# Optimization experiments

Measured on AMD Instinct MI355X. Metric: run time of the kernel, lower is better.

The kernel has to match this reference:

```python
import jax, jax.numpy as jnp
import numpy as np


def setup_inputs() -> dict:
    key = jax.random.key(0)
    ks = jax.random.split(key, 6)
    N, E, D = 50000, 500000, 128
    H, O = 256, 128
    x = jax.random.normal(ks[0], (N, D), dtype=jnp.float32)
    edge_attr = jax.random.normal(ks[1], (E, D), dtype=jnp.float32)
    edge_index = jax.random.randint(ks[2], (E, 2), 0, N, dtype=jnp.int64)
    # MLP params, scaled like torch default init
    W1 = jax.random.normal(ks[3], (3 * D, H), dtype=jnp.float32) / np.sqrt(3 * D)
    b1 = jnp.zeros((H,), dtype=jnp.float32)
    W2 = jax.random.normal(ks[4], (H, O), dtype=jnp.float32) / np.sqrt(H)
    b2 = jnp.zeros((O,), dtype=jnp.float32)
    return {"x": x, "edge_attr": edge_attr, "W1": W1, "b1": b1,
            "W2": W2, "b2": b2, "edge_index": edge_index}


def reference(x, edge_attr, W1, b1, W2, b2, edge_index):
    # edge_index: [E, 2]; column 0 = sender, column 1 = receiver
    sender = x[edge_index[:, 0]]    # [E, D] gather
    receiver = x[edge_index[:, 1]]  # [E, D] gather
    feat = jnp.concatenate([sender, receiver, edge_attr], axis=-1)  # [E, 3D]
    h = jax.nn.relu(feat @ W1 + b1)  # [E, H]
    return h @ W2 + b2               # [E, O]
```

## Files before the change

kernel.cpp:

```cpp
#include <hip/hip_runtime.h>
#include <hip/hip_bf16.h>

#define D 128
#define K1 384
#define H 256
#define O 128
#define BE 64
#define GRIDP 256
#define LDF (K1 + 8)
#define LDHF (H + 8)

typedef __attribute__((ext_vector_type(8))) short bf16x8;
typedef __attribute__((ext_vector_type(4))) float f32x4;

#define SSW(row, col) ((row) * 128 + ((col) ^ (((row) & 15) << 3)))
#define HSW(row, col) ((row) * 256 + ((col) ^ (((row) & 15) << 3)))

#define LGKM_BARRIER()                                                 \
    do {                                                               \
        asm volatile("s_waitcnt lgkmcnt(0)\n\ts_barrier" ::: "memory");\
        __builtin_amdgcn_sched_barrier(0);                             \
    } while (0)

__device__ inline ushort f2b(float f) {
    union { float f; unsigned u; } v; v.f = f;
    unsigned u = v.u;
    unsigned r = (u + 0x7fffu + ((u >> 16) & 1u)) >> 16;
    return (ushort)r;
}
__device__ inline ushort4 cvt4(float4 v) {
    ushort4 u; u.x = f2b(v.x); u.y = f2b(v.y); u.z = f2b(v.z); u.w = f2b(v.w); return u;
}
__device__ inline unsigned cvtpk(float lo, float hi) {
    unsigned r;
    asm("v_cvt_pk_bf16_f32 %0, %1, %2" : "=v"(r) : "v"(lo), "v"(hi));
    return r;
}
__device__ inline bf16x8 cvt8(f32x4 a, f32x4 b) {
    union { bf16x8 v; unsigned w[4]; } u;
    u.w[0] = cvtpk(a[0], a[1]); u.w[1] = cvtpk(a[2], a[3]);
    u.w[2] = cvtpk(b[0], b[1]); u.w[3] = cvtpk(b[2], b[3]);
    return u.v;
}

__global__ void prep_weights(const float* __restrict__ W1, const float* __restrict__ W2,
                             ushort* __restrict__ W1t, ushort* __restrict__ W2t) {
    int tid = blockIdx.x * blockDim.x + threadIdx.x;
    if (tid < 256 * 384) {
        int n = tid / 384, k = tid % 384;
        W1t[tid] = f2b(W1[k * 256 + n]);
    } else {
        int t2 = tid - 256 * 384;
        if (t2 < 128 * 256) {
            int o = t2 / 256, k = t2 % 256;
            W2t[t2] = f2b(W2[k * 128 + o]);
        }
    }
}

__global__ __launch_bounds__(256)
void prep_x(const float* __restrict__ x, ushort* __restrict__ Xb, long total8) {
    long t = (long)blockIdx.x * blockDim.x + threadIdx.x;
    if (t < total8) {
        const float* src = x + t * 8;
        float4 v0 = ((const float4*)src)[0], v1 = ((const float4*)src)[1];
        union { bf16x8 v; ushort4 u[2]; } w;
        w.u[0] = cvt4(v0); w.u[1] = cvt4(v1);
        *(bf16x8*)(Xb + t * 8) = w.v;
    }
}

__global__ __launch_bounds__(512, 2)
void edge_mlp16(const float* __restrict__ ea, const int* __restrict__ eidx,
                const ushort* __restrict__ Xb,
                const ushort* __restrict__ W1t, const ushort* __restrict__ W2t,
                const float* __restrict__ b1, const float* __restrict__ b2,
                float* __restrict__ out, int E, int ntiles) {
    __shared__ __align__(16) ushort sBuf[65536];
    ushort* sH = sBuf + 49152;

    const int tid = threadIdx.x;
    const int wave = tid >> 6, lane = tid & 63;
    const int row16 = lane & 15, kgrp = lane >> 4;
    const int srow = tid >> 3, oct = tid & 7;

    bf16x8 w1f[12][2];
    #pragma unroll
    for (int ks = 0; ks < 12; ++ks)
        #pragma unroll
        for (int fc = 0; fc < 2; ++fc)
            w1f[ks][fc] = *(const bf16x8*)(W1t + (wave * 32 + fc * 16 + row16) * K1 + ks * 32 + kgrp * 8);
    bf16x8 w2f[8];
    #pragma unroll
    for (int ks = 0; ks < 8; ++ks)
        w2f[ks] = *(const bf16x8*)(W2t + (wave * 16 + row16) * H + ks * 32 + kgrp * 8);
    float4 b1q[2];
    #pragma unroll
    for (int fc = 0; fc < 2; ++fc)
        b1q[fc] = *(const float4*)(b1 + wave * 32 + fc * 16 + kgrp * 4);
    const float b2v = b2[wave * 16 + row16];

    int t = blockIdx.x;
    if (t >= ntiles) return;

    bf16x8 pxs[2], pxr[2];
    f32x4  pea[4];

    {
        long se = (long)t * BE + srow; if (se >= E) se = E - 1;
        int2 ei = *(const int2*)(eidx + 2 * se);
        const ushort* ps = Xb + (long)ei.x * D + oct * 16;
        const ushort* pr = Xb + (long)ei.y * D + oct * 16;
        const float*  pe = ea + se * D + oct * 16;
        #pragma unroll
        for (int j = 0; j < 2; ++j) pxs[j] = *(const bf16x8*)(ps + j * 8);
        #pragma unroll
        for (int j = 0; j < 2; ++j) pxr[j] = *(const bf16x8*)(pr + j * 8);
        #pragma unroll
        for (int j = 0; j < 4; ++j) pea[j] = ((const f32x4*)pe)[j];

        #pragma unroll
        for (int j = 0; j < 2; ++j) *(bf16x8*)(sBuf + SSW(srow, oct * 16 + j * 8)) = pxs[j];
        #pragma unroll
        for (int j = 0; j < 2; ++j) *(bf16x8*)(sBuf + 8192 + SSW(srow, oct * 16 + j * 8)) = pxr[j];
        *(bf16x8*)(sBuf + 16384 + SSW(srow, oct * 16 + 0)) = cvt8(pea[0], pea[1]);
        *(bf16x8*)(sBuf + 16384 + SSW(srow, oct * 16 + 8)) = cvt8(pea[2], pea[3]);
    }

    int p = 0;
    int tprev = -1;
    int tn = t + GRIDP;
    int2 ei2;
    {
        int tc = (tn < ntiles) ? tn : (ntiles - 1);
        long se = (long)tc * BE + srow; if (se >= E) se = E - 1;
        ei2 = *(const int2*)(eidx + 2 * se);
    }

    for (;;) {
        LGKM_BARRIER();
        const bool hasNext = (tn < ntiles);

        if (tprev >= 0) {
            f32x4 acc2[4];
            #pragma unroll
            for (int fr = 0; fr < 4; ++fr) acc2[fr] = (f32x4){0,0,0,0};
            #pragma unroll
            for (int ks = 0; ks < 8; ++ks) {
                bf16x8 a[4];
                #pragma unroll
                for (int fr = 0; fr < 4; ++fr)
                    a[fr] = *(const bf16x8*)(sH + HSW(fr * 16 + row16, ks * 32 + kgrp * 8));
                #pragma unroll
                for (int fr = 0; fr < 4; ++fr)
                    acc2[fr] = __builtin_amdgcn_mfma_f32_16x16x32_bf16(a[fr], w2f[ks], acc2[fr], 0, 0, 0);
            }
            const long e0p = (long)tprev * BE;
            #pragma unroll
            for (int fr = 0; fr < 4; ++fr)
                #pragma unroll
                for (int r = 0; r < 4; ++r) {
                    long erow = e0p + fr * 16 + kgrp * 4 + r;
                    if (erow < E) out[erow * O + wave * 16 + row16] = acc2[fr][r] + b2v;
                }
        }

        if (hasNext) {
            long sen = (long)tn * BE + srow; if (sen >= E) sen = E - 1;
            const ushort* ps = Xb + (long)ei2.x * D + oct * 16;
            const ushort* pr = Xb + (long)ei2.y * D + oct * 16;
            const float*  pe = ea + sen * D + oct * 16;
            #pragma unroll
            for (int j = 0; j < 2; ++j) pxs[j] = *(const bf16x8*)(ps + j * 8);
            #pragma unroll
            for (int j = 0; j < 2; ++j) pxr[j] = *(const bf16x8*)(pr + j * 8);
            #pragma unroll
            for (int j = 0; j < 4; ++j) pea[j] = ((const f32x4*)pe)[j];
            int tnn = tn + GRIDP;
            int tc = (tnn < ntiles) ? tnn : (ntiles - 1);
            long se2 = (long)tc * BE + srow; if (se2 >= E) se2 = E - 1;
            ei2 = *(const int2*)(eidx + 2 * se2);
        }

        const ushort* sA = sBuf + (p ? 24576 : 0);
        f32x4 acc[4][2];
        #pragma unroll
        for (int fe = 0; fe < 4; ++fe) { acc[fe][0] = (f32x4){0,0,0,0}; acc[fe][1] = (f32x4){0,0,0,0}; }
        #pragma unroll
        for (int ks = 0; ks < 12; ++ks) {
            const ushort* sP = sA + ((ks < 4) ? 0 : ((ks < 8) ? 8192 : 16384));
            const int kl = (ks & 3) * 32 + kgrp * 8;
            bf16x8 a[4];
            #pragma unroll
            for (int fe = 0; fe < 4; ++fe)
                a[fe] = *(const bf16x8*)(sP + SSW(fe * 16 + row16, kl));
            #pragma unroll
            for (int fe = 0; fe < 4; ++fe) {
                acc[fe][0] = __builtin_amdgcn_mfma_f32_16x16x32_bf16(w1f[ks][0], a[fe], acc[fe][0], 0, 0, 0);
                acc[fe][1] = __builtin_amdgcn_mfma_f32_16x16x32_bf16(w1f[ks][1], a[fe], acc[fe][1], 0, 0, 0);
            }
        }

        if (hasNext) {
            ushort* sB = sBuf + (p ? 0 : 24576);
            #pragma unroll
            for (int j = 0; j < 2; ++j) *(bf16x8*)(sB + SSW(srow, oct * 16 + j * 8)) = pxs[j];
            #pragma unroll
            for (int j = 0; j < 2; ++j) *(bf16x8*)(sB + 8192 + SSW(srow, oct * 16 + j * 8)) = pxr[j];
            *(bf16x8*)(sB + 16384 + SSW(srow, oct * 16 + 0)) = cvt8(pea[0], pea[1]);
            *(bf16x8*)(sB + 16384 + SSW(srow, oct * 16 + 8)) = cvt8(pea[2], pea[3]);
        }

        LGKM_BARRIER();

        #pragma unroll
        for (int fe = 0; fe < 4; ++fe) {
            int erow = fe * 16 + row16;
            int base = erow * 256;
            int swz = (erow & 15) << 3;
            #pragma unroll
            for (int fc = 0; fc < 2; ++fc) {
                int colb = wave * 32 + fc * 16 + kgrp * 4;
                union { uint2 w; ushort4 u; } pk;
                pk.w.x = cvtpk(fmaxf(acc[fe][fc][0] + b1q[fc].x, 0.f),
                               fmaxf(acc[fe][fc][1] + b1q[fc].y, 0.f));
                pk.w.y = cvtpk(fmaxf(acc[fe][fc][2] + b1q[fc].z, 0.f),
                               fmaxf(acc[fe][fc][3] + b1q[fc].w, 0.f));
                *(ushort4*)(sH + base + (colb ^ swz)) = pk.u;
            }
        }

        tprev = t; t = tn; tn += GRIDP;
        if (t >= ntiles) break;
        p ^= 1;
    }

    LGKM_BARRIER();
    {
        f32x4 acc2[4];
        #pragma unroll
        for (int fr = 0; fr < 4; ++fr) acc2[fr] = (f32x4){0,0,0,0};
        #pragma unroll
        for (int ks = 0; ks < 8; ++ks) {
            bf16x8 a[4];
            #pragma unroll
            for (int fr = 0; fr < 4; ++fr)
                a[fr] = *(const bf16x8*)(sH + HSW(fr * 16 + row16, ks * 32 + kgrp * 8));
            #pragma unroll
            for (int fr = 0; fr < 4; ++fr)
                acc2[fr] = __builtin_amdgcn_mfma_f32_16x16x32_bf16(a[fr], w2f[ks], acc2[fr], 0, 0, 0);
        }
        const long e0p = (long)tprev * BE;
        #pragma unroll
        for (int fr = 0; fr < 4; ++fr)
            #pragma unroll
            for (int r = 0; r < 4; ++r) {
                long erow = e0p + fr * 16 + kgrp * 4 + r;
                if (erow < E) out[erow * O + wave * 16 + row16] = acc2[fr][r] + b2v;
            }
    }
}

__global__ __launch_bounds__(256, 2)
void edge_mlp(const float* __restrict__ x, const float* __restrict__ ea,
              const int* __restrict__ eidx,
              const float* __restrict__ b1, const float* __restrict__ b2,
              const ushort* __restrict__ W1t, const ushort* __restrict__ W2t,
              float* __restrict__ out, int E) {
    __shared__ ushort sF[64 * LDF];
    ushort* sH = sF;
    const int tid = threadIdx.x, wave = tid >> 6, lane = tid & 63;
    const int row16 = lane & 15, kgrp = lane >> 4;
    const long e0 = (long)blockIdx.x * 64;
    {
        int i = tid >> 2, p = tid & 3;
        long e = e0 + i; if (e >= E) e = E - 1;
        int s = eidx[2 * e], r = eidx[2 * e + 1];
        const float* src0 = x + (long)s * D + p * 32;
        const float* src1 = x + (long)r * D + p * 32;
        const float* src2 = ea + e * D + p * 32;
        ushort* dst = sF + i * LDF + p * 32;
        #pragma unroll
        for (int j = 0; j < 8; ++j) *(ushort4*)(dst + 0 * D + j * 4) = cvt4(((const float4*)src0)[j]);
        #pragma unroll
        for (int j = 0; j < 8; ++j) *(ushort4*)(dst + 1 * D + j * 4) = cvt4(((const float4*)src1)[j]);
        #pragma unroll
        for (int j = 0; j < 8; ++j) *(ushort4*)(dst + 2 * D + j * 4) = cvt4(((const float4*)src2)[j]);
    }
    __syncthreads();
    f32x4 acc[4][4];
    #pragma unroll
    for (int a = 0; a < 4; ++a)
        #pragma unroll
        for (int b = 0; b < 4; ++b) acc[a][b] = (f32x4){0,0,0,0};
    const int wcol = wave * 64;
    for (int k0 = 0; k0 < K1; k0 += 32) {
        bf16x8 a[4], b[4];
        #pragma unroll
        for (int fr = 0; fr < 4; ++fr)
            a[fr] = *(const bf16x8*)(sF + (fr * 16 + row16) * LDF + k0 + kgrp * 8);
        #pragma unroll
        for (int fc = 0; fc < 4; ++fc)
            b[fc] = *(const bf16x8*)(W1t + (wcol + fc * 16 + row16) * K1 + k0 + kgrp * 8);
        #pragma unroll
        for (int fr = 0; fr < 4; ++fr)
            #pragma unroll
            for (int fc = 0; fc < 4; ++fc)
                acc[fr][fc] = __builtin_amdgcn_mfma_f32_16x16x32_bf16(a[fr], b[fc], acc[fr][fc], 0, 0, 0);
    }
    __syncthreads();
    #pragma unroll
    for (int fc = 0; fc < 4; ++fc) {
        int col = wcol + fc * 16 + row16;
        float bv = b1[col];
        #pragma unroll
        for (int fr = 0; fr < 4; ++fr)
            #pragma unroll
            for (int r = 0; r < 4; ++r) {
                int row = fr * 16 + kgrp * 4 + r;
                sH[row * LDHF + col] = f2b(fmaxf(acc[fr][fc][r] + bv, 0.f));
            }
    }
    __syncthreads();
    f32x4 acc2[4][2];
    #pragma unroll
    for (int a = 0; a < 4; ++a)
        #pragma unroll
        for (int b = 0; b < 2; ++b) acc2[a][b] = (f32x4){0,0,0,0};
    const int wo = wave * 32;
    for (int k0 = 0; k0 < H; k0 += 32) {
        bf16x8 a[4], b[2];
        #pragma unroll
        for (int fr = 0; fr < 4; ++fr)
            a[fr] = *(const bf16x8*)(sH + (fr * 16 + row16) * LDHF + k0 + kgrp * 8);
        #pragma unroll
        for (int fc = 0; fc < 2; ++fc)
            b[fc] = *(const bf16x8*)(W2t + (wo + fc * 16 + row16) * H + k0 + kgrp * 8);
        #pragma unroll
        for (int fr = 0; fr < 4; ++fr)
            #pragma unroll
            for (int fc = 0; fc < 2; ++fc)
                acc2[fr][fc] = __builtin_amdgcn_mfma_f32_16x16x32_bf16(a[fr], b[fc], acc2[fr][fc], 0, 0, 0);
    }
    #pragma unroll
    for (int fc = 0; fc < 2; ++fc) {
        int col = wo + fc * 16 + row16;
        float bv = b2[col];
        #pragma unroll
        for (int fr = 0; fr < 4; ++fr)
            #pragma unroll
            for (int r = 0; r < 4; ++r) {
                long row = e0 + fr * 16 + kgrp * 4 + r;
                if (row < E) out[row * O + col] = acc2[fr][fc][r] + bv;
            }
    }
}

extern "C" void kernel_launch(void* const* d_in, const int* in_sizes, int n_in,
                              void* d_out, int out_size, void* d_ws, size_t ws_size,
                              hipStream_t stream) {
    const float* x  = (const float*)d_in[0];
    const float* ea = (const float*)d_in[1];
    const float* W1 = (const float*)d_in[2];
    const float* b1 = (const float*)d_in[3];
    const float* W2 = (const float*)d_in[4];
    const float* b2 = (const float*)d_in[5];
    const int* eidx = (const int*)d_in[6];
    float* out = (float*)d_out;

    const int E = in_sizes[1] / D;
    const int N = in_sizes[0] / D;

    ushort* W1t = (ushort*)d_ws;
    ushort* W2t = W1t + 256 * 384;
    ushort* Xb  = W2t + 128 * 256;
    size_t need = ((size_t)(256 * 384 + 128 * 256) + (size_t)N * 128) * 2;

    prep_weights<<<512, 256, 0, stream>>>(W1, W2, W1t, W2t);

    if (ws_size >= need) {
        long total8 = (long)N * D / 8;
        int nbx = (int)((total8 + 255) / 256);
        prep_x<<<nbx, 256, 0, stream>>>(x, Xb, total8);
        int ntiles = (E + BE - 1) / BE;
        int grid = (ntiles < GRIDP) ? ntiles : GRIDP;
        edge_mlp16<<<grid, 512, 0, stream>>>(ea, eidx, Xb, W1t, W2t, b1, b2, out, E, ntiles);
    } else {
        int nb = (E + 63) / 64;
        edge_mlp<<<nb, 256, 0, stream>>>(x, ea, eidx, b1, b2, W1t, W2t, out, E);
    }
}
```

Measured before the change: 190.1 us.

## Load gathered node rows directly from global into MFMA operands, skip LDS staging

Sender and receiver bf16 node rows are no longer prefetched into double-buffered LDS tiles. Each wave now loads them straight from global memory as MFMA B-operands, using per-lane edge indices fetched in the current iteration. Only edge_attr stays staged in LDS, which cuts the shared buffer from 128KB to 64KB and removes the LDS writes and reads for the gathered rows. In exchange, the gather latency now sits on the critical path of the first GEMM instead of being overlapped with the previous tile, and every wave repeats the same gather loads.

Result: slower. 357.1 us (+87.8%).

```diff
diff --git a/kernel.cpp b/kernel.cpp
--- a/kernel.cpp
+++ b/kernel.cpp
@@ -71,13 +71,13 @@
 }
 
 __global__ __launch_bounds__(512, 2)
-void edge_mlp16(const float* __restrict__ ea, const int* __restrict__ eidx,
+void edge_mlp17(const float* __restrict__ ea, const int* __restrict__ eidx,
                 const ushort* __restrict__ Xb,
                 const ushort* __restrict__ W1t, const ushort* __restrict__ W2t,
                 const float* __restrict__ b1, const float* __restrict__ b2,
                 float* __restrict__ out, int E, int ntiles) {
-    __shared__ __align__(16) ushort sBuf[65536];
-    ushort* sH = sBuf + 49152;
+    __shared__ __align__(16) ushort sBuf[32768];
+    ushort* sH = sBuf + 16384;
 
     const int tid = threadIdx.x;
     const int wave = tid >> 6, lane = tid & 63;
@@ -103,39 +103,20 @@
     int t = blockIdx.x;
     if (t >= ntiles) return;
 
-    bf16x8 pxs[2], pxr[2];
-    f32x4  pea[4];
+    f32x4 pea[4];
 
     {
         long se = (long)t * BE + srow; if (se >= E) se = E - 1;
-        int2 ei = *(const int2*)(eidx + 2 * se);
-        const ushort* ps = Xb + (long)ei.x * D + oct * 16;
-        const ushort* pr = Xb + (long)ei.y * D + oct * 16;
-        const float*  pe = ea + se * D + oct * 16;
-        #pragma unroll
-        for (int j = 0; j < 2; ++j) pxs[j] = *(const bf16x8*)(ps + j * 8);
-        #pragma unroll
-        for (int j = 0; j < 2; ++j) pxr[j] = *(const bf16x8*)(pr + j * 8);
+        const float* pe = ea + se * D + oct * 16;
         #pragma unroll
         for (int j = 0; j < 4; ++j) pea[j] = ((const f32x4*)pe)[j];
-
-        #pragma unroll
-        for (int j = 0; j < 2; ++j) *(bf16x8*)(sBuf + SSW(srow, oct * 16 + j * 8)) = pxs[j];
-        #pragma unroll
-        for (int j = 0; j < 2; ++j) *(bf16x8*)(sBuf + 8192 + SSW(srow, oct * 16 + j * 8)) = pxr[j];
-        *(bf16x8*)(sBuf + 16384 + SSW(srow, oct * 16 + 0)) = cvt8(pea[0], pea[1]);
-        *(bf16x8*)(sBuf + 16384 + SSW(srow, oct * 16 + 8)) = cvt8(pea[2], pea[3]);
+        *(bf16x8*)(sBuf + SSW(srow, oct * 16 + 0)) = cvt8(pea[0], pea[1]);
+        *(bf16x8*)(sBuf + SSW(srow, oct * 16 + 8)) = cvt8(pea[2], pea[3]);
     }
 
     int p = 0;
     int tprev = -1;
     int tn = t + GRIDP;
-    int2 ei2;
-    {
-        int tc = (tn < ntiles) ? tn : (ntiles - 1);
-        long se = (long)tc * BE + srow; if (se >= E) se = E - 1;
-        ei2 = *(const int2*)(eidx + 2 * se);
-    }
 
     for (;;) {
         LGKM_BARRIER();
@@ -167,48 +148,69 @@
 
         if (hasNext) {
             long sen = (long)tn * BE + srow; if (sen >= E) sen = E - 1;
-            const ushort* ps = Xb + (long)ei2.x * D + oct * 16;
-            const ushort* pr = Xb + (long)ei2.y * D + oct * 16;
-            const float*  pe = ea + sen * D + oct * 16;
-            #pragma unroll
-            for (int j = 0; j < 2; ++j) pxs[j] = *(const bf16x8*)(ps + j * 8);
-            #pragma unroll
-            for (int j = 0; j < 2; ++j) pxr[j] = *(const bf16x8*)(pr + j * 8);
+            const float* pe = ea + sen * D + oct * 16;
             #pragma unroll
             for (int j = 0; j < 4; ++j) pea[j] = ((const f32x4*)pe)[j];
-            int tnn = tn + GRIDP;
-            int tc = (tnn < ntiles) ? tnn : (ntiles - 1);
-            long se2 = (long)tc * BE + srow; if (se2 >= E) se2 = E - 1;
-            ei2 = *(const int2*)(eidx + 2 * se2);
-        }
-
-        const ushort* sA = sBuf + (p ? 24576 : 0);
+        }
+
+        int2 ei[4];
+        {
+            const long e0 = (long)t * BE;
+            #pragma unroll
+            for (int fe = 0; fe < 4; ++fe) {
+                long e = e0 + fe * 16 + row16; if (e >= E) e = E - 1;
+                ei[fe] = *(const int2*)(eidx + 2 * e);
+            }
+        }
         f32x4 acc[4][2];
         #pragma unroll
         for (int fe = 0; fe < 4; ++fe) { acc[fe][0] = (f32x4){0,0,0,0}; acc[fe][1] = (f32x4){0,0,0,0}; }
-        #pragma unroll
-        for (int ks = 0; ks < 12; ++ks) {
-            const ushort* sP = sA + ((ks < 4) ? 0 : ((ks < 8) ? 8192 : 16384));
-            const int kl = (ks & 3) * 32 + kgrp * 8;
+
+        #pragma unroll
+        for (int ks = 0; ks < 4; ++ks) {
             bf16x8 a[4];
             #pragma unroll
             for (int fe = 0; fe < 4; ++fe)
-                a[fe] = *(const bf16x8*)(sP + SSW(fe * 16 + row16, kl));
+                a[fe] = *(const bf16x8*)(Xb + (long)ei[fe].x * D + ks * 32 + kgrp * 8);
             #pragma unroll
             for (int fe = 0; fe < 4; ++fe) {
                 acc[fe][0] = __builtin_amdgcn_mfma_f32_16x16x32_bf16(w1f[ks][0], a[fe], acc[fe][0], 0, 0, 0);
                 acc[fe][1] = __builtin_amdgcn_mfma_f32_16x16x32_bf16(w1f[ks][1], a[fe], acc[fe][1], 0, 0, 0);
             }
         }
+        #pragma unroll
+        for (int ks = 0; ks < 4; ++ks) {
+            bf16x8 a[4];
+            #pragma unroll
+            for (int fe = 0; fe < 4; ++fe)
+                a[fe] = *(const bf16x8*)(Xb + (long)ei[fe].y * D + ks * 32 + kgrp * 8);
+            #pragma unroll
+            for (int fe = 0; fe < 4; ++fe) {
+                acc[fe][0] = __builtin_amdgcn_mfma_f32_16x16x32_bf16(w1f[4 + ks][0], a[fe], acc[fe][0], 0, 0, 0);
+                acc[fe][1] = __builtin_amdgcn_mfma_f32_16x16x32_bf16(w1f[4 + ks][1], a[fe], acc[fe][1], 0, 0, 0);
+            }
+        }
+        {
+            const ushort* sEA = sBuf + (p ? 8192 : 0);
+            #pragma unroll
+            for (int ks = 0; ks < 4; ++ks) {
+                const int kl = ks * 32 + kgrp * 8;
+                bf16x8 a[4];
+                #pragma unroll
+                for (int fe = 0; fe < 4; ++fe)
+                    a[fe] = *(const bf16x8*)(sEA + SSW(fe * 16 + row16, kl));
+                #pragma unroll
+                for (int fe = 0; fe < 4; ++fe) {
+                    acc[fe][0] = __builtin_amdgcn_mfma_f32_16x16x32_bf16(w1f[8 + ks][0], a[fe], acc[fe][0], 0, 0, 0);
+                    acc[fe][1] = __builtin_amdgcn_mfma_f32_16x16x32_bf16(w1f[8 + ks][1], a[fe], acc[fe][1], 0, 0, 0);
+                }
+            }
+        }
 
         if (hasNext) {
-            ushort* sB = sBuf + (p ? 0 : 24576);
-            #pragma unroll
-            for (int j = 0; j < 2; ++j) *(bf16x8*)(sB + SSW(srow, oct * 16 + j * 8)) = pxs[j];
-            #pragma unroll
-            for (int j = 0; j < 2; ++j) *(bf16x8*)(sB + 8192 + SSW(srow, oct * 16 + j * 8)) = pxr[j];
-            *(bf16x8*)(sB + 16384 + SSW(srow, oct * 16 + 0)) = cvt8(pea[0], pea[1]);
-            *(bf16x8*)(sB + 16384 + SSW(srow, oct * 16 + 8)) = cvt8(pea[2], pea[3]);
+            ushort* sB = sBuf + (p ? 0 : 8192);
+            *(bf16x8*)(sB + SSW(srow, oct * 16 + 0)) = cvt8(pea[0], pea[1]);
+            *(bf16x8*)(sB + SSW(srow, oct * 16 + 8)) = cvt8(pea[2], pea[3]);
         }
 
         LGKM_BARRIER();
@@ -384,7 +386,7 @@
         prep_x<<<nbx, 256, 0, stream>>>(x, Xb, total8);
         int ntiles = (E + BE - 1) / BE;
         int grid = (ntiles < GRIDP) ? ntiles : GRIDP;
-        edge_mlp16<<<grid, 512, 0, stream>>>(ea, eidx, Xb, W1t, W2t, b1, b2, out, E, ntiles);
+        edge_mlp17<<<grid, 512, 0, stream>>>(ea, eidx, Xb, W1t, W2t, b1, b2, out, E, ntiles);
     } else {
         int nb = (E + 63) / 64;
         edge_mlp<<<nb, 256, 0, stream>>>(x, ea, eidx, b1, b2, W1t, W2t, out, E);
```
